# Optimization experiments

Hardware: AMD Instinct MI355X
Metric: run time of the kernel (lower is better)

The kernel has to match this reference:

```python
import jax, jax.numpy as jnp
import numpy as np

N = 50000      # nodes
E = 1000000    # edges
R = 16         # relations
NB = 16        # bases = min(30, R)
D = 128        # entity/hidden/output dim
V = 500000     # entities
L = 3          # layers
G = 64         # graphs in batch
EPS = 1e-5


def setup_inputs() -> dict:
    key = jax.random.key(0)
    ks = jax.random.split(key, 11)
    node_ids = jax.random.randint(ks[0], (N,), 0, V)
    edge_index = jax.random.randint(ks[1], (2, E), 0, N)
    edge_type = jax.random.randint(ks[2], (E,), 0, R)
    batch = jnp.sort(jax.random.randint(ks[3], (N,), 0, G))
    emb = (jax.random.normal(ks[4], (V, D), jnp.float32) * 0.02).at[0].set(0.0)  # padding_idx=0
    comp = jax.random.normal(ks[5], (L, R, NB), jnp.float32) / np.sqrt(NB).astype(np.float32)
    basis = jax.random.normal(ks[6], (L, NB, D, D), jnp.float32) / np.sqrt(D).astype(np.float32)
    root = jax.random.normal(ks[7], (L, D, D), jnp.float32) / np.sqrt(D).astype(np.float32)
    bias = jnp.zeros((L, D), jnp.float32)
    gamma = jnp.ones((L, D), jnp.float32)
    beta = jnp.zeros((L, D), jnp.float32)
    return {"node_ids": node_ids, "edge_index": edge_index, "edge_type": edge_type,
            "batch": batch, "emb": emb, "comp": comp, "basis": basis, "root": root,
            "bias": bias, "gamma": gamma, "beta": beta}


def _rgcn_layer(x, src, dst, seg, comp_l, basis_l, root_l, bias_l, inv_cnt):
    # Per-relation mean aggregation: mean-then-transform == transform-then-mean (linear).
    msum = jax.ops.segment_sum(x[src], seg, num_segments=N * R)       # [N*R, D]
    mean = (msum * inv_cnt).reshape(N, R, -1)                          # [N, R, D]
    W = jnp.einsum('rb,bio->rio', comp_l, basis_l)                     # [R, D, D]
    return jnp.einsum('nri,rio->no', mean, W) + x @ root_l + bias_l


def _layernorm(x, g, b):
    mu = jnp.mean(x, axis=-1, keepdims=True)
    var = jnp.mean(jnp.square(x - mu), axis=-1, keepdims=True)
    return (x - mu) * jax.lax.rsqrt(var + EPS) * g + b


def reference(node_ids, edge_index, edge_type, batch, emb, comp, basis, root, bias, gamma, beta):
    src, dst = edge_index[0], edge_index[1]
    seg = dst * R + edge_type                                          # [(node, relation)] segment id
    cnt = jax.ops.segment_sum(jnp.ones((E,), jnp.float32), seg, num_segments=N * R)
    inv_cnt = (1.0 / jnp.maximum(cnt, 1.0))[:, None]                   # [N*R, 1]
    x = emb[node_ids]                                                  # [N, D]
    for l in range(L):
        x_new = _rgcn_layer(x, src, dst, seg, comp[l], basis[l], root[l], bias[l], inv_cnt)
        x_new = jax.nn.relu(_layernorm(x_new, gamma[l], beta[l]))      # dropout = identity (eval)
        x = x + x_new                                                  # dims match every layer
    gsum = jax.ops.segment_sum(x, batch, num_segments=G)               # global_mean_pool
    gcnt = jax.ops.segment_sum(jnp.ones((N,), jnp.float32), batch, num_segments=G)
    graph_embedding = gsum / jnp.maximum(gcnt, 1.0)[:, None]
    return x, graph_embedding
```

## Files before the change

kernel.cpp:

```cpp
#include <hip/hip_runtime.h>
#include <hip/hip_bf16.h>

#define N_ 50000
#define E_ 1000000
#define R_ 16
#define NB_ 16
#define D_ 128
#define L_ 3
#define G_ 64
#define M_SEG (N_*R_)
#define KTOT ((R_+1)*D_)
#define SCAN_BLOCKS ((M_SEG + 1023)/1024)
#define MAXM 450000
#define GM 128
#define LDSB 136

typedef _Float16 f16;
typedef _Float16 f16x8 __attribute__((ext_vector_type(8)));
typedef _Float16 f16x4 __attribute__((ext_vector_type(4)));
typedef _Float16 f16x2 __attribute__((ext_vector_type(2)));
typedef float f32x4 __attribute__((ext_vector_type(4)));


__global__ __launch_bounds__(256) void k_hist(const int* __restrict__ ei, const int* __restrict__ et,
                                              int* __restrict__ cnt){
  int e = blockIdx.x*256 + threadIdx.x;
  if (e < E_){
    int seg = ei[E_ + e]*R_ + et[e];
    atomicAdd(&cnt[seg], 1);
  }
}

__global__ __launch_bounds__(256) void k_scan_sum(const int* __restrict__ cnt, int* __restrict__ bsum){
  __shared__ int sh[256];
  int base = blockIdx.x*1024 + threadIdx.x*4;
  int s = 0;
  #pragma unroll
  for (int j=0;j<4;++j){ int i = base + j; if (i < M_SEG) s += cnt[i]; }
  sh[threadIdx.x] = s; __syncthreads();
  for (int off=128; off>0; off>>=1){
    if (threadIdx.x < off) sh[threadIdx.x] += sh[threadIdx.x+off];
    __syncthreads();
  }
  if (threadIdx.x==0) bsum[blockIdx.x] = sh[0];
}

__global__ __launch_bounds__(256) void k_scan_off(const int* __restrict__ bsum, int* __restrict__ boff){
  __shared__ int sh[256];
  int tid = threadIdx.x;
  int v[4]; int ts = 0;
  #pragma unroll
  for (int j=0;j<4;++j){ int i = tid*4+j; v[j] = (i<SCAN_BLOCKS)? bsum[i] : 0; ts += v[j]; }
  sh[tid] = ts; __syncthreads();
  for (int off=1; off<256; off<<=1){
    int a = sh[tid];
    int b = (tid>=off)? sh[tid-off] : 0;
    __syncthreads(); sh[tid] = a + b; __syncthreads();
  }
  int excl = sh[tid] - ts;
  #pragma unroll
  for (int j=0;j<4;++j){ int i = tid*4+j; if (i<SCAN_BLOCKS) boff[i] = excl; excl += v[j]; }
}

__global__ __launch_bounds__(256) void k_scan_write(const int* __restrict__ cnt, const int* __restrict__ boff,
                                                    int* __restrict__ row_ptr, int* __restrict__ cursor,
                                                    float* __restrict__ inv){
  __shared__ int sh[256];
  int tid = threadIdx.x;
  int base = blockIdx.x*1024 + tid*4;
  int v[4]; int ts = 0;
  #pragma unroll
  for (int j=0;j<4;++j){ int i = base+j; v[j] = (i<M_SEG)? cnt[i] : 0; ts += v[j]; }
  sh[tid] = ts; __syncthreads();
  for (int off=1; off<256; off<<=1){
    int a = sh[tid];
    int b = (tid>=off)? sh[tid-off] : 0;
    __syncthreads(); sh[tid] = a + b; __syncthreads();
  }
  int excl = boff[blockIdx.x] + sh[tid] - ts;
  #pragma unroll
  for (int j=0;j<4;++j){
    int i = base+j;
    if (i < M_SEG){
      row_ptr[i] = excl; cursor[i] = excl;
      int c = v[j];
      inv[i] = 1.0f / (float)(c > 1 ? c : 1);
      if (i == M_SEG-1) row_ptr[M_SEG] = excl + c;
    }
    excl += v[j];
  }
}

__global__ __launch_bounds__(256) void k_place(const int* __restrict__ ei, const int* __restrict__ et,
                                               int* __restrict__ cursor, int* __restrict__ csr_src){
  int e = blockIdx.x*256 + threadIdx.x;
  if (e < E_){
    int seg = ei[E_+e]*R_ + et[e];
    int pos = atomicAdd(&cursor[seg], 1);
    csr_src[pos] = ei[e];
  }
}

__global__ __launch_bounds__(256) void k_idx(const int* __restrict__ cnt, const int* __restrict__ row_ptr,
                                             const int* __restrict__ csr_src,
                                             int* __restrict__ idxT, int* __restrict__ mlist,
                                             int* __restrict__ mcount){
  int i = blockIdx.x*256 + threadIdx.x;
  if (i < M_SEG){
    int n = i >> 4, r = i & 15;
    int c = cnt[i];
    int v;
    if (c == 0) v = 1;
    else if (c == 1) v = csr_src[row_ptr[i]] << 1;
    else {
      int slot = atomicAdd(mcount, 1);
      if (slot < MAXM){ mlist[slot] = i; v = ((1 + slot) << 1) | 1; }
      else v = 1;
    }
    idxT[r*N_ + n] = v;
  } else if (i < M_SEG + N_){
    int n = i - M_SEG;
    idxT[16*N_ + n] = n << 1;
  }
}


__global__ __launch_bounds__(128) void k_gather(const int* __restrict__ ids, const float* __restrict__ emb,
                                                float* __restrict__ x, f16* __restrict__ x16){
  int t = threadIdx.x;
  int n = blockIdx.x*4 + (t >> 5);
  int c = (t & 31) * 4;
  if (n < N_){
    int id = ids[n];
    float4 v = *(const float4*)(emb + (size_t)id*D_ + c);
    *(float4*)(x + (size_t)n*D_ + c) = v;
    f16x4 h = {(f16)v.x, (f16)v.y, (f16)v.z, (f16)v.w};
    *(f16x4*)(x16 + (size_t)n*D_ + c) = h;
  }
}

__global__ __launch_bounds__(128) void k_wprep(const float* __restrict__ comp, const float* __restrict__ basis,
                                               const float* __restrict__ root, f16* __restrict__ Wt){
  int b = blockIdx.x;
  int o = threadIdx.x;
  int l = b / ((R_+1)*D_);
  int rem = b % ((R_+1)*D_);
  int r = rem / D_;
  int i = rem % D_;
  float acc = 0.f;
  if (r < R_){
    #pragma unroll
    for (int bb=0; bb<NB_; ++bb)
      acc += comp[(l*R_+r)*NB_+bb] * basis[((l*NB_+bb)*D_+i)*D_+o];
  } else {
    acc = root[(l*D_+i)*D_+o];
  }
  Wt[(size_t)l*D_*KTOT + (size_t)o*KTOT + r*D_ + i] = (f16)acc;
}

__global__ __launch_bounds__(256) void k_means(const f16* __restrict__ x16,
                                               const int* __restrict__ row_ptr, const int* __restrict__ csr_src,
                                               const float* __restrict__ inv,
                                               const int* __restrict__ mlist, const int* __restrict__ mcount,
                                               f16* __restrict__ abuf){
  int gw = (blockIdx.x*256 + threadIdx.x) >> 6;
  int lane = threadIdx.x & 63;
  int mc = *mcount; if (mc > MAXM) mc = MAXM;
  int nw = gridDim.x * 4;
  for (int slot = gw; slot < mc; slot += nw){
    int seg = mlist[slot];
    int p0 = row_ptr[seg], p1 = row_ptr[seg+1];
    float a0 = 0.f, a1 = 0.f;
    for (int p = p0; p < p1; ++p){
      int src = csr_src[p];
      f16x2 v = *(const f16x2*)(x16 + (size_t)src*D_ + lane*2);
      a0 += (float)v[0]; a1 += (float)v[1];
    }
    float ic = inv[seg];
    f16x2 o = {(f16)(a0*ic), (f16)(a1*ic)};
    *(f16x2*)(abuf + (size_t)(1+slot)*D_ + lane*2) = o;
  }
}

__global__ __launch_bounds__(256) void k_gemm(
    const int* __restrict__ idxT, const f16* __restrict__ x16, const f16* __restrict__ abuf,
    const f16* __restrict__ Wt, const float* __restrict__ xin,
    const float* __restrict__ bias, const float* __restrict__ gamma, const float* __restrict__ beta,
    float* __restrict__ xout, f16* __restrict__ xout16)
{
  __shared__ __align__(16) f16 bsl[D_][LDSB];

  const int tid  = threadIdx.x;
  const int lane = tid & 63;
  const int wave = tid >> 6;
  const int l15  = lane & 15;
  const int quad = lane >> 4;
  const int nbase = blockIdx.x * GM;

  f32x4 acc[2][8];
  f32x4 z = {0.f,0.f,0.f,0.f};
  #pragma unroll
  for (int h=0;h<2;++h)
    #pragma unroll
    for (int nt=0;nt<8;++nt) acc[h][nt] = z;

  int nodeh[2];
  #pragma unroll
  for (int h=0;h<2;++h) nodeh[h] = nbase + (wave*2 + h)*16 + l15;

  const int so = tid >> 4;
  const int sk = (tid & 15) * 8;

  for (int r = 0; r < R_+1; ++r){
    __syncthreads();
    #pragma unroll
    for (int oo = 0; oo < 8; ++oo){
      int orow = oo*16 + so;
      f16x8 w = *(const f16x8*)(Wt + (size_t)orow*KTOT + r*D_ + sk);
      *(f16x8*)&bsl[orow][sk] = w;
    }
    __syncthreads();

    const f16* ab[2];
    #pragma unroll
    for (int h=0;h<2;++h){
      int node = nodeh[h];
      int aidx = (node < N_) ? idxT[r*N_ + node] : 1;
      ab[h] = ((aidx & 1) ? abuf : x16) + (size_t)(aidx >> 1) * D_;
    }

    #pragma unroll
    for (int ks = 0; ks < 4; ++ks){
      f16x8 af0 = *(const f16x8*)(ab[0] + ks*32 + quad*8);
      f16x8 af1 = *(const f16x8*)(ab[1] + ks*32 + quad*8);
      #pragma unroll
      for (int nt = 0; nt < 8; ++nt){
        f16x8 bf = *(const f16x8*)&bsl[nt*16 + l15][ks*32 + quad*8];
        acc[0][nt] = __builtin_amdgcn_mfma_f32_16x16x32_f16(af0, bf, acc[0][nt], 0, 0, 0);
        acc[1][nt] = __builtin_amdgcn_mfma_f32_16x16x32_f16(af1, bf, acc[1][nt], 0, 0, 0);
      }
    }
  }

  float bv[8], gv[8], btv[8];
  #pragma unroll
  for (int nt=0;nt<8;++nt){
    int col = nt*16 + l15;
    bv[nt] = bias[col]; gv[nt] = gamma[col]; btv[nt] = beta[col];
  }
  #pragma unroll
  for (int h=0;h<2;++h){
    #pragma unroll
    for (int j=0;j<4;++j){
      int rowl = (wave*2 + h)*16 + quad*4 + j;
      int node = nbase + rowl;
      float t[8]; float s=0.f, s2=0.f;
      #pragma unroll
      for (int nt=0;nt<8;++nt){
        float v = acc[h][nt][j] + bv[nt];
        t[nt] = v; s += v; s2 += v*v;
      }
      #pragma unroll
      for (int m=1;m<16;m<<=1){ s += __shfl_xor(s,m,64); s2 += __shfl_xor(s2,m,64); }
      float mu  = s * (1.f/128.f);
      float var = s2 * (1.f/128.f) - mu*mu;
      float rs  = rsqrtf(var + 1e-5f);
      if (node < N_){
        #pragma unroll
        for (int nt=0;nt<8;++nt){
          int col = nt*16 + l15;
          float o = (t[nt]-mu)*rs*gv[nt] + btv[nt];
          o = fmaxf(o, 0.f);
          float res = xin[(size_t)node*D_ + col] + o;
          xout[(size_t)node*D_ + col] = res;
          xout16[(size_t)node*D_ + col] = (f16)res;
        }
      }
    }
  }
}


__device__ __forceinline__ int lbound_batch(const int* __restrict__ b, int key){
  int lo=0, hi=N_;
  while (lo<hi){ int mid=(lo+hi)>>1; if (b[mid]<key) lo=mid+1; else hi=mid; }
  return lo;
}

__global__ __launch_bounds__(256) void k_pool(const float* __restrict__ x, const int* __restrict__ batch,
                                              float* __restrict__ gout){
  __shared__ float sh[256];
  int g = blockIdx.x;
  int a = lbound_batch(batch, g);
  int b = lbound_batch(batch, g+1);
  int t = threadIdx.x;
  int d = t & 127, half = t >> 7;
  float s = 0.f;
  for (int n = a + half; n < b; n += 2) s += x[(size_t)n*D_ + d];
  sh[t] = s; __syncthreads();
  if (half == 0){
    float tot = sh[t] + sh[t+128];
    int c = b - a;
    gout[g*D_ + d] = tot / (float)(c > 1 ? c : 1);
  }
}


extern "C" void kernel_launch(void* const* d_in, const int* in_sizes, int n_in,
                              void* d_out, int out_size, void* d_ws, size_t ws_size,
                              hipStream_t stream){
  const int*   node_ids = (const int*)d_in[0];
  const int*   ei       = (const int*)d_in[1];
  const int*   et       = (const int*)d_in[2];
  const int*   batch    = (const int*)d_in[3];
  const float* emb      = (const float*)d_in[4];
  const float* comp     = (const float*)d_in[5];
  const float* basis    = (const float*)d_in[6];
  const float* root     = (const float*)d_in[7];
  const float* bias     = (const float*)d_in[8];
  const float* gamma    = (const float*)d_in[9];
  const float* beta     = (const float*)d_in[10];
  float* out = (float*)d_out;

  char* ws = (char*)d_ws;
  size_t off = 0;
  auto alloc = [&](size_t bytes) -> void* {
    void* p = ws + off;
    off = (off + bytes + 255) & ~(size_t)255;
    return p;
  };
  int*   cnt     = (int*)  alloc((size_t)M_SEG*4);
  int*   row_ptr = (int*)  alloc(((size_t)M_SEG+1)*4);
  int*   cursor  = (int*)  alloc((size_t)M_SEG*4);
  float* invc    = (float*)alloc((size_t)M_SEG*4);
  int*   csr_src = (int*)  alloc((size_t)E_*4);
  int*   bsum    = (int*)  alloc((size_t)SCAN_BLOCKS*4);
  int*   boff    = (int*)  alloc((size_t)SCAN_BLOCKS*4);
  int*   idxT    = (int*)  alloc((size_t)(R_+1)*N_*4);
  int*   mlist   = (int*)  alloc((size_t)MAXM*4);
  int*   mcount  = (int*)  alloc(256);
  float* xA      = (float*)alloc((size_t)N_*D_*4);
  float* xB      = (float*)alloc((size_t)N_*D_*4);
  f16*   xA16    = (f16*)  alloc((size_t)N_*D_*2);
  f16*   xB16    = (f16*)  alloc((size_t)N_*D_*2);
  f16*   Wt      = (f16*)  alloc((size_t)L_*D_*KTOT*2);
  f16*   abuf    = (f16*)  alloc((size_t)(MAXM+1)*D_*2);

  hipMemsetAsync(cnt, 0, (size_t)M_SEG*4, stream);
  hipMemsetAsync(mcount, 0, 256, stream);
  hipMemsetAsync(abuf, 0, (size_t)D_*2, stream);

  k_hist      <<<(E_+255)/256, 256, 0, stream>>>(ei, et, cnt);
  k_scan_sum  <<<SCAN_BLOCKS, 256, 0, stream>>>(cnt, bsum);
  k_scan_off  <<<1, 256, 0, stream>>>(bsum, boff);
  k_scan_write<<<SCAN_BLOCKS, 256, 0, stream>>>(cnt, boff, row_ptr, cursor, invc);
  k_place     <<<(E_+255)/256, 256, 0, stream>>>(ei, et, cursor, csr_src);
  k_idx       <<<(M_SEG+N_+255)/256, 256, 0, stream>>>(cnt, row_ptr, csr_src, idxT, mlist, mcount);
  k_gather    <<<(N_+3)/4, 128, 0, stream>>>(node_ids, emb, xA, xA16);
  k_wprep     <<<L_*(R_+1)*D_, 128, 0, stream>>>(comp, basis, root, Wt);

  const int GB = (N_ + GM - 1)/GM;
  k_means<<<4096, 256, 0, stream>>>(xA16, row_ptr, csr_src, invc, mlist, mcount, abuf);
  k_gemm <<<GB, 256, 0, stream>>>(idxT, xA16, abuf, Wt + (size_t)0*D_*KTOT, xA,
                                  bias+0*D_, gamma+0*D_, beta+0*D_, xB, xB16);
  k_means<<<4096, 256, 0, stream>>>(xB16, row_ptr, csr_src, invc, mlist, mcount, abuf);
  k_gemm <<<GB, 256, 0, stream>>>(idxT, xB16, abuf, Wt + (size_t)1*D_*KTOT, xB,
                                  bias+1*D_, gamma+1*D_, beta+1*D_, xA, xA16);
  k_means<<<4096, 256, 0, stream>>>(xA16, row_ptr, csr_src, invc, mlist, mcount, abuf);
  k_gemm <<<GB, 256, 0, stream>>>(idxT, xA16, abuf, Wt + (size_t)2*D_*KTOT, xA,
                                  bias+2*D_, gamma+2*D_, beta+2*D_, out, xB16);

  k_pool <<<G_, 256, 0, stream>>>(out, batch, out + (size_t)N_*D_);
}
```

Measured before the change: 1.236 ms.

## Read GEMM weights directly from global, prefetch indices, widen mean gather

The GEMM kernel no longer stages weight tiles through shared memory with two barriers per relation. Each lane now loads its B fragments straight from global memory (expected to hit in L2/L1) and prefetches the next relation's gather index. The mean kernel gives each segment a 32-lane group instead of a 64-lane wave, loads 4 halves per lane, and unrolls by two edges for more memory-level parallelism. The cost is redundant global weight loads across waves and less reuse than the LDS tile offered.

```diff
diff --git a/kernel.cpp b/kernel.cpp
--- a/kernel.cpp
+++ b/kernel.cpp
@@ -13,12 +13,10 @@
 #define SCAN_BLOCKS ((M_SEG + 1023)/1024)
 #define MAXM 450000
 #define GM 128
-#define LDSB 136
 
 typedef _Float16 f16;
 typedef _Float16 f16x8 __attribute__((ext_vector_type(8)));
 typedef _Float16 f16x4 __attribute__((ext_vector_type(4)));
-typedef _Float16 f16x2 __attribute__((ext_vector_type(2)));
 typedef float f32x4 __attribute__((ext_vector_type(4)));
 
 
@@ -163,22 +161,31 @@
                                                const float* __restrict__ inv,
                                                const int* __restrict__ mlist, const int* __restrict__ mcount,
                                                f16* __restrict__ abuf){
-  int gw = (blockIdx.x*256 + threadIdx.x) >> 6;
-  int lane = threadIdx.x & 63;
+  int grp = (blockIdx.x*256 + threadIdx.x) >> 5;
+  int l32 = threadIdx.x & 31;
   int mc = *mcount; if (mc > MAXM) mc = MAXM;
-  int nw = gridDim.x * 4;
-  for (int slot = gw; slot < mc; slot += nw){
+  int ngrp = gridDim.x * 8;
+  for (int slot = grp; slot < mc; slot += ngrp){
     int seg = mlist[slot];
     int p0 = row_ptr[seg], p1 = row_ptr[seg+1];
-    float a0 = 0.f, a1 = 0.f;
-    for (int p = p0; p < p1; ++p){
-      int src = csr_src[p];
-      f16x2 v = *(const f16x2*)(x16 + (size_t)src*D_ + lane*2);
-      a0 += (float)v[0]; a1 += (float)v[1];
+    float a0=0.f,a1=0.f,a2=0.f,a3=0.f;
+    float b0=0.f,b1=0.f,b2=0.f,b3=0.f;
+    int p = p0;
+    for (; p + 1 < p1; p += 2){
+      int s0 = csr_src[p], s1 = csr_src[p+1];
+      f16x4 v0 = *(const f16x4*)(x16 + (size_t)s0*D_ + l32*4);
+      f16x4 v1 = *(const f16x4*)(x16 + (size_t)s1*D_ + l32*4);
+      a0 += (float)v0[0]; a1 += (float)v0[1]; a2 += (float)v0[2]; a3 += (float)v0[3];
+      b0 += (float)v1[0]; b1 += (float)v1[1]; b2 += (float)v1[2]; b3 += (float)v1[3];
+    }
+    if (p < p1){
+      int s0 = csr_src[p];
+      f16x4 v0 = *(const f16x4*)(x16 + (size_t)s0*D_ + l32*4);
+      a0 += (float)v0[0]; a1 += (float)v0[1]; a2 += (float)v0[2]; a3 += (float)v0[3];
     }
     float ic = inv[seg];
-    f16x2 o = {(f16)(a0*ic), (f16)(a1*ic)};
-    *(f16x2*)(abuf + (size_t)(1+slot)*D_ + lane*2) = o;
+    f16x4 o = {(f16)((a0+b0)*ic), (f16)((a1+b1)*ic), (f16)((a2+b2)*ic), (f16)((a3+b3)*ic)};
+    *(f16x4*)(abuf + (size_t)(1+slot)*D_ + l32*4) = o;
   }
 }
 
@@ -188,8 +195,6 @@
     const float* __restrict__ bias, const float* __restrict__ gamma, const float* __restrict__ beta,
     float* __restrict__ xout, f16* __restrict__ xout16)
 {
-  __shared__ __align__(16) f16 bsl[D_][LDSB];
-
   const int tid  = threadIdx.x;
   const int lane = tid & 63;
   const int wave = tid >> 6;
@@ -208,38 +213,39 @@
   #pragma unroll
   for (int h=0;h<2;++h) nodeh[h] = nbase + (wave*2 + h)*16 + l15;
 
-  const int so = tid >> 4;
-  const int sk = (tid & 15) * 8;
+  const f16* wp[8];
+  #pragma unroll
+  for (int nt=0;nt<8;++nt)
+    wp[nt] = Wt + (size_t)(nt*16 + l15)*KTOT + quad*8;
+
+  int aidx[2];
+  #pragma unroll
+  for (int h=0;h<2;++h) aidx[h] = (nodeh[h] < N_) ? idxT[nodeh[h]] : 1;
 
   for (int r = 0; r < R_+1; ++r){
-    __syncthreads();
-    #pragma unroll
-    for (int oo = 0; oo < 8; ++oo){
-      int orow = oo*16 + so;
-      f16x8 w = *(const f16x8*)(Wt + (size_t)orow*KTOT + r*D_ + sk);
-      *(f16x8*)&bsl[orow][sk] = w;
-    }
-    __syncthreads();
-
     const f16* ab[2];
     #pragma unroll
-    for (int h=0;h<2;++h){
-      int node = nodeh[h];
-      int aidx = (node < N_) ? idxT[r*N_ + node] : 1;
-      ab[h] = ((aidx & 1) ? abuf : x16) + (size_t)(aidx >> 1) * D_;
+    for (int h=0;h<2;++h)
+      ab[h] = ((aidx[h] & 1) ? abuf : x16) + (size_t)(aidx[h] >> 1) * D_ + quad*8;
+
+    if (r < R_){
+      #pragma unroll
+      for (int h=0;h<2;++h) aidx[h] = (nodeh[h] < N_) ? idxT[(r+1)*N_ + nodeh[h]] : 1;
     }
 
     #pragma unroll
     for (int ks = 0; ks < 4; ++ks){
-      f16x8 af0 = *(const f16x8*)(ab[0] + ks*32 + quad*8);
-      f16x8 af1 = *(const f16x8*)(ab[1] + ks*32 + quad*8);
+      f16x8 af0 = *(const f16x8*)(ab[0] + ks*32);
+      f16x8 af1 = *(const f16x8*)(ab[1] + ks*32);
       #pragma unroll
       for (int nt = 0; nt < 8; ++nt){
-        f16x8 bf = *(const f16x8*)&bsl[nt*16 + l15][ks*32 + quad*8];
+        f16x8 bf = *(const f16x8*)(wp[nt] + ks*32);
         acc[0][nt] = __builtin_amdgcn_mfma_f32_16x16x32_f16(af0, bf, acc[0][nt], 0, 0, 0);
         acc[1][nt] = __builtin_amdgcn_mfma_f32_16x16x32_f16(af1, bf, acc[1][nt], 0, 0, 0);
       }
     }
+    #pragma unroll
+    for (int nt=0;nt<8;++nt) wp[nt] += D_;
   }
 
   float bv[8], gv[8], btv[8];
```

New measurement: 1.315 ms. 1.06x slower.
